# Kernel tuning notes

Measured on AMD Instinct MI355X. Metric: run time of the kernel, lower is better.

Reference implementation:

```python
import jax, jax.numpy as jnp
import numpy as np

B, D, N, MH, MV = 4, 1024, 2048, 1024, 1024

def setup_inputs() -> dict:
    key = jax.random.key(0)
    k1, k2, k3, k4, k5 = jax.random.split(key, 5)
    return {
        "x": jax.random.normal(k1, (B, D, N), dtype=jnp.float32),
        "W_Q": jax.random.normal(k2, (MH, D), dtype=jnp.float32),
        "W_K": jax.random.normal(k3, (MH, D), dtype=jnp.float32),
        "W_V": jax.random.normal(k4, (MV, D), dtype=jnp.float32),
        "W_O": jax.random.normal(k5, (D, MV), dtype=jnp.float32),
    }

def reference(x, W_Q, W_K, W_V, W_O):
    # x: [b, d, n] (feature-major). Projections: [b, m, n]
    q = jnp.einsum('hd,bdn->bhn', W_Q, x)
    k = jnp.einsum('hd,bdn->bhn', W_K, x)
    v = jnp.einsum('vd,bdn->bvn', W_V, x)
    # scores[b,i,j] = sum_h k[b,h,i] * q[b,h,j]  -> [b, n, n]; NOTE: no 1/sqrt scale (faithful)
    scores = jnp.einsum('bhi,bhj->bij', k, q)
    scores = jax.nn.softmax(scores, axis=-1)
    # v @ scores -> [b, m_V, n]
    attn = jnp.einsum('bvi,bij->bvj', v, scores)
    # W_O @ attn -> [b, d, n]
    return jnp.einsum('dv,bvj->bdj', W_O, attn)
```

## Files before the change

kernel.cpp:

```cpp
#include <hip/hip_runtime.h>
#include <cstddef>
#include <cstdint>

typedef unsigned short u16;
typedef __attribute__((ext_vector_type(8))) short bf16x8;
typedef __attribute__((ext_vector_type(8))) _Float16 f16x8;
typedef __attribute__((ext_vector_type(4))) float f32x4;
typedef __attribute__((ext_vector_type(16))) float f32x16;

#define GLOBAL_AS __attribute__((address_space(1)))
#define LDS_AS __attribute__((address_space(3)))

__device__ __forceinline__ void async16(const u16* g, u16* l) {
    __builtin_amdgcn_global_load_lds((GLOBAL_AS const uint32_t*)g,
                                     (LDS_AS uint32_t*)l, 16, 0, 0);
}

__device__ __forceinline__ u16 f2bf(float f) {
    uint32_t u = __builtin_bit_cast(uint32_t, f);
    uint32_t r = (u + 0x7FFFu + ((u >> 16) & 1u)) >> 16;
    return (u16)r;
}

__global__ __launch_bounds__(256)
void wprep(const float* __restrict__ WQ, const float* __restrict__ WK,
           const float* __restrict__ WV, const float* __restrict__ WO,
           u16* __restrict__ DQ, u16* __restrict__ DK,
           u16* __restrict__ DV, u16* __restrict__ DOb)
{
    const int role = blockIdx.z;
    __shared__ float t[32][33];
    int tx = threadIdx.x & 31, ty = threadIdx.x >> 5;
    int c0 = blockIdx.x * 32, r0 = blockIdx.y * 32;
    const float* S = role == 0 ? WQ : role == 1 ? WK : role == 2 ? WV : WO;

    if (role == 3) {
        #pragma unroll
        for (int k = 0; k < 4; ++k) {
            size_t o = (size_t)(r0 + ty + 8 * k) * 1024 + c0 + tx;
            DOb[o] = f2bf(S[o]);
        }
        return;
    }
    #pragma unroll
    for (int k = 0; k < 4; ++k)
        t[ty + 8 * k][tx] = S[(size_t)(r0 + ty + 8 * k) * 1024 + c0 + tx];
    __syncthreads();
    if (role == 2) {
        #pragma unroll
        for (int k = 0; k < 4; ++k)
            DV[(size_t)(c0 + ty + 8 * k) * 1024 + r0 + tx] = f2bf(t[tx][ty + 8 * k]);
    } else {
        u16* D = role == 0 ? DQ : DK;
        #pragma unroll
        for (int k = 0; k < 4; ++k) {
            float a = t[tx][ty + 8 * k] * 64.0f;
            _Float16 h0 = (_Float16)a;
            _Float16 h1 = (_Float16)(a - (float)h0);
            size_t o = (size_t)(c0 + ty + 8 * k) * 1024 + r0 + tx;
            D[o] = __builtin_bit_cast(u16, h0);
            D[1048576 + o] = __builtin_bit_cast(u16, h1);
        }
    }
}

__global__ __launch_bounds__(256)
void xprep(const float* __restrict__ Sb, size_t sBatch,
           u16* __restrict__ BFb, size_t bfBatch,
           u16* __restrict__ Db, size_t dBatch, size_t plane)
{
    const float* S = Sb + blockIdx.z * sBatch;
    u16* BF = BFb + blockIdx.z * bfBatch;
    u16* D = Db + blockIdx.z * dBatch;
    __shared__ float t[32][33];
    int tx = threadIdx.x & 31, ty = threadIdx.x >> 5;
    int c0 = blockIdx.x * 32, r0 = blockIdx.y * 32;
    #pragma unroll
    for (int k = 0; k < 4; ++k) {
        float v = S[(size_t)(r0 + ty + 8 * k) * 2048 + c0 + tx];
        t[ty + 8 * k][tx] = v;
        BF[(size_t)(r0 + ty + 8 * k) * 2048 + c0 + tx] = f2bf(v);
    }
    __syncthreads();
    #pragma unroll
    for (int k = 0; k < 4; ++k) {
        float a = t[tx][ty + 8 * k] * 64.0f;
        _Float16 h0 = (_Float16)a;
        _Float16 h1 = (_Float16)(a - (float)h0);
        size_t o = (size_t)(c0 + ty + 8 * k) * 1024 + r0 + tx;
        D[o] = __builtin_bit_cast(u16, h0);
        D[plane + o] = __builtin_bit_cast(u16, h1);
    }
}

#define MMF4(AF, BF)                                                                   \
    _Pragma("unroll") for (int i = 0; i < 4; ++i)                                      \
        _Pragma("unroll") for (int j = 0; j < 4; ++j)                                  \
            acc[i][j] = __builtin_amdgcn_mfma_f32_16x16x32_f16(AF[i], BF[j], acc[i][j], 0, 0, 0);
#define MMB4(AF, BF)                                                                   \
    _Pragma("unroll") for (int i = 0; i < 4; ++i)                                      \
        _Pragma("unroll") for (int j = 0; j < 4; ++j)                                  \
            acc[i][j] = __builtin_amdgcn_mfma_f32_16x16x32_bf16(AF[i], BF[j], acc[i][j], 0, 0, 0);

template<int TERMS, int SPLITK>
__global__ __launch_bounds__(256)
void gemm_big(const u16* __restrict__ Ab, size_t aPlane,
              const u16* __restrict__ Bb, size_t bPlane,
              float* __restrict__ Cb, size_t cBatch,
              int M, int N, int K)
{
    constexpr int RSZ = 4096;
    constexpr int BUF = (TERMS == 3 ? 4 : 2) * RSZ;
    __shared__ u16 lds[2 * BUF];
    const u16* A = Ab;
    const u16* B = Bb;
    const int z = blockIdx.z;
    const int kt0 = SPLITK ? z * (K >> 2) : 0;
    const int kend = SPLITK ? kt0 + (K >> 2) : K;
    const int tid = threadIdx.x;
    const int lane = tid & 63, wave = tid >> 6;
    const int m0 = blockIdx.y * 128, n0 = blockIdx.x * 128;
    const int l15 = lane & 15, q = lane >> 4;
    const int rm = (wave >> 1) * 64, rn = (wave & 1) * 64;

    int sr[2], sg[2], sbase[2];
    #pragma unroll
    for (int it = 0; it < 2; ++it) {
        int s = tid + it * 256;
        sr[it] = s >> 2;
        sg[it] = (s & 3) ^ ((sr[it] >> 1) & 3);
        sbase[it] = (it * 256 + wave * 64) * 8;
    }
    const int fsw = (q ^ ((l15 >> 1) & 3)) * 8;
    int aoff[4], boff[4];
    #pragma unroll
    for (int f = 0; f < 4; ++f) {
        aoff[f] = (rm + f * 16 + l15) * 32 + fsw;
        boff[f] = (rn + f * 16 + l15) * 32 + fsw;
    }

    f32x4 acc[4][4];
    #pragma unroll
    for (int i = 0; i < 4; ++i)
        #pragma unroll
        for (int j = 0; j < 4; ++j)
            acc[i][j] = (f32x4){0.f, 0.f, 0.f, 0.f};

#define STAGEB(PP, KT)                                                                 \
    do {                                                                               \
        _Pragma("unroll")                                                              \
        for (int it = 0; it < 2; ++it) {                                               \
            const size_t ao = (size_t)(m0 + sr[it]) * K + (KT) + sg[it] * 8;           \
            const size_t bo = (size_t)(n0 + sr[it]) * K + (KT) + sg[it] * 8;           \
            const int d = (PP) * BUF + sbase[it];                                      \
            if (TERMS == 3) {                                                          \
                async16(A + ao, &lds[d]);                                              \
                async16(A + aPlane + ao, &lds[d + RSZ]);                               \
                async16(B + bo, &lds[d + 2 * RSZ]);                                    \
                async16(B + bPlane + bo, &lds[d + 3 * RSZ]);                           \
            } else {                                                                   \
                async16(A + ao, &lds[d]);                                              \
                async16(B + bo, &lds[d + RSZ]);                                        \
            }                                                                          \
        }                                                                              \
    } while (0)

    STAGEB(0, kt0);
    for (int kt = kt0; kt < kend; kt += 32) {
        const int p = (kt >> 5) & 1;
        __syncthreads();
        if (kt + 32 < kend) STAGEB(p ^ 1, kt + 32);
        const u16* L = &lds[p * BUF];
        if (TERMS == 3) {
            f16x8 a0f[4], b0f[4], xf[4];
            #pragma unroll
            for (int f = 0; f < 4; ++f) a0f[f] = *(const f16x8*)&L[aoff[f]];
            #pragma unroll
            for (int f = 0; f < 4; ++f) b0f[f] = *(const f16x8*)&L[2 * RSZ + boff[f]];
            MMF4(a0f, b0f);
            #pragma unroll
            for (int f = 0; f < 4; ++f) xf[f] = *(const f16x8*)&L[3 * RSZ + boff[f]];
            MMF4(a0f, xf);
            #pragma unroll
            for (int f = 0; f < 4; ++f) xf[f] = *(const f16x8*)&L[RSZ + aoff[f]];
            MMF4(xf, b0f);
        } else {
            bf16x8 af[4], bf_[4];
            #pragma unroll
            for (int f = 0; f < 4; ++f) af[f] = *(const bf16x8*)&L[aoff[f]];
            #pragma unroll
            for (int f = 0; f < 4; ++f) bf_[f] = *(const bf16x8*)&L[RSZ + boff[f]];
            MMB4(af, bf_);
        }
    }
#undef STAGEB

    float* C = Cb + (size_t)z * cBatch;
    #pragma unroll
    for (int i = 0; i < 4; ++i) {
        int row = m0 + rm + i * 16 + q * 4;
        #pragma unroll
        for (int j = 0; j < 4; ++j) {
            int col = n0 + rn + j * 16 + l15;
            #pragma unroll
            for (int r = 0; r < 4; ++r)
                C[(size_t)(row + r) * N + col] = acc[i][j][r];
        }
    }
}

__global__ __launch_bounds__(256)
void reduce4b(const float4* __restrict__ P1, const float4* __restrict__ P2,
              u16* __restrict__ M2, u16* __restrict__ WOV)
{
    size_t i = blockIdx.x * 256 + threadIdx.x;
    const float4* P = blockIdx.y == 0 ? P1 : P2;
    float4 a = P[i], b = P[262144 + i], c = P[524288 + i], d = P[786432 + i];
    float v[4] = { a.x + b.x + c.x + d.x, a.y + b.y + c.y + d.y,
                   a.z + b.z + c.z + d.z, a.w + b.w + c.w + d.w };
    if (blockIdx.y == 0) {
        #pragma unroll
        for (int k = 0; k < 4; ++k) {
            float vs = v[k] * 0.000244140625f;
            _Float16 h0 = (_Float16)vs;
            _Float16 h1 = (_Float16)(vs - (float)h0);
            M2[i * 4 + k] = __builtin_bit_cast(u16, h0);
            M2[1048576 + i * 4 + k] = __builtin_bit_cast(u16, h1);
        }
    } else {
        ushort4 o = { f2bf(v[0]), f2bf(v[1]), f2bf(v[2]), f2bf(v[3]) };
        *(ushort4*)&WOV[i * 4] = o;
    }
}

#define RDAF(dst, PL, H)                                                               \
    _Pragma("unroll")                                                                  \
    for (int f = 0; f < FM; ++f)                                                       \
        dst[f] = *(const f16x8*)&L[(PL) * ASZ + arow[f] * 32 + ((2 * (H) + half) ^ asw[f]) * 8];
#define RDBF(dst, PL, H)                                                               \
    _Pragma("unroll")                                                                  \
    for (int f = 0; f < FN; ++f)                                                       \
        dst[f] = *(const f16x8*)&L[2 * ASZ + (PL) * BSZ + brow[f] * 32 + ((2 * (H) + half) ^ bsw[f]) * 8];
#define MMW(AF, BF)                                                                    \
    _Pragma("unroll")                                                                  \
    for (int i = 0; i < FM; ++i)                                                       \
        _Pragma("unroll")                                                              \
        for (int j = 0; j < FN; ++j)                                                   \
            acc[i][j] = __builtin_amdgcn_mfma_f32_32x32x16_f16(AF[i], BF[j], acc[i][j], 0, 0, 0);
#define MMWB(AF, BF)                                                                   \
    _Pragma("unroll")                                                                  \
    for (int i = 0; i < FM; ++i)                                                       \
        _Pragma("unroll")                                                              \
        for (int j = 0; j < FN; ++j)                                                   \
            acc[i][j] = __builtin_amdgcn_mfma_f32_32x32x16_bf16(AF[i], BF[j], acc[i][j], 0, 0, 0);

template<int TERMS, int EPI, int TM, int TN, int WGM, int WGN>
__global__ __launch_bounds__(512, 2)
void gemm_w(const u16* __restrict__ Ab, size_t aBatch, size_t aPlane,
            const u16* __restrict__ Bb, size_t bBatch, size_t bPlane,
            void* __restrict__ Cb, size_t cBatch, size_t cPlane,
            int M, int N, int K)
{
    constexpr int ASZ = TM * 32;
    constexpr int BSZ = TN * 32;
    constexpr int APL = (TERMS == 3) ? 2 : 1;
    constexpr int BUF = APL * (ASZ + BSZ);
    constexpr int FM = TM / WGM / 32;
    constexpr int FN = TN / WGN / 32;
    constexpr int AIT = TM / 128;
    constexpr int BIT = TN / 128;
    extern __shared__ __align__(16) u16 lds[];

    int bid = blockIdx.x + gridDim.x * blockIdx.y;
    int cpr = gridDim.x >> 2;
    int c8 = bid & 7, kk = bid >> 3;
    int bx = (kk % cpr) * 4 + (c8 & 3);
    int by = (kk / cpr) * 2 + (c8 >> 2);

    const u16* A = Ab + blockIdx.z * aBatch;
    const u16* B = Bb + blockIdx.z * bBatch;
    const int tid = threadIdx.x;
    const int lane = tid & 63, wave = tid >> 6;
    const int m0 = by * TM, n0 = bx * TN;
    const int l31 = lane & 31, half = lane >> 5;
    const int rm = (wave / WGN) * (TM / WGM);
    const int rn = (wave % WGN) * (TN / WGN);

    int arow[FM], asw[FM], brow[FN], bsw[FN];
    #pragma unroll
    for (int f = 0; f < FM; ++f) { arow[f] = rm + f * 32 + l31; asw[f] = (arow[f] >> 1) & 3; }
    #pragma unroll
    for (int f = 0; f < FN; ++f) { brow[f] = rn + f * 32 + l31; bsw[f] = (brow[f] >> 1) & 3; }

    f32x16 acc[FM][FN];
    #pragma unroll
    for (int i = 0; i < FM; ++i)
        #pragma unroll
        for (int j = 0; j < FN; ++j)
            #pragma unroll
            for (int r = 0; r < 16; ++r) acc[i][j][r] = 0.f;

    auto stage = [&](int pp, int kt) {
        #pragma unroll
        for (int it = 0; it < AIT; ++it) {
            int s = tid + it * 512;
            int r = s >> 2;
            int g = (s & 3) ^ ((r >> 1) & 3);
            int base = pp * BUF + (it * 512 + wave * 64) * 8;
            size_t go = (size_t)(m0 + r) * K + kt + g * 8;
            async16(A + go, &lds[base]);
            if (TERMS == 3) async16(A + aPlane + go, &lds[base + ASZ]);
        }
        #pragma unroll
        for (int it = 0; it < BIT; ++it) {
            int s = tid + it * 512;
            int r = s >> 2;
            int g = (s & 3) ^ ((r >> 1) & 3);
            int base = pp * BUF + APL * ASZ + (it * 512 + wave * 64) * 8;
            size_t go = (size_t)(n0 + r) * K + kt + g * 8;
            async16(B + go, &lds[base]);
            if (TERMS == 3) async16(B + bPlane + go, &lds[base + BSZ]);
        }
    };

    stage(0, 0);
    for (int kt = 0; kt < K; kt += 32) {
        const int p = (kt >> 5) & 1;
        __syncthreads();
        if (kt + 32 < K) stage(p ^ 1, kt + 32);
        const u16* L = &lds[p * BUF];
        if (TERMS == 3) {
            f16x8 A0h0[FM], A0h1[FM], B0h0[FN], B0h1[FN];
            f16x8 B1h0[FN], B1h1[FN], A1h0[FM], A1h1[FM];
            RDAF(A0h0, 0, 0) RDBF(B0h0, 0, 0)
            RDAF(A0h1, 0, 1) RDBF(B0h1, 0, 1)
            RDBF(B1h0, 1, 0)
            MMW(A0h0, B0h0)
            RDBF(B1h1, 1, 1)
            MMW(A0h1, B0h1)
            RDAF(A1h0, 1, 0)
            MMW(A0h0, B1h0)
            MMW(A0h1, B1h1)
            RDAF(A1h1, 1, 1)
            MMW(A1h0, B0h0)
            MMW(A1h1, B0h1)
        } else {
            bf16x8 Ah0[FM], Ah1[FM], Bh0[FN], Bh1[FN];
            #pragma unroll
            for (int f = 0; f < FM; ++f)
                Ah0[f] = *(const bf16x8*)&L[arow[f] * 32 + (half ^ asw[f]) * 8];
            #pragma unroll
            for (int f = 0; f < FN; ++f)
                Bh0[f] = *(const bf16x8*)&L[ASZ + brow[f] * 32 + (half ^ bsw[f]) * 8];
            #pragma unroll
            for (int f = 0; f < FM; ++f)
                Ah1[f] = *(const bf16x8*)&L[arow[f] * 32 + ((2 + half) ^ asw[f]) * 8];
            #pragma unroll
            for (int f = 0; f < FN; ++f)
                Bh1[f] = *(const bf16x8*)&L[ASZ + brow[f] * 32 + ((2 + half) ^ bsw[f]) * 8];
            MMWB(Ah0, Bh0)
            MMWB(Ah1, Bh1)
        }
    }

    #pragma unroll
    for (int i = 0; i < FM; ++i) {
        #pragma unroll
        for (int j = 0; j < FN; ++j) {
            int col = n0 + rn + j * 32 + l31;
            #pragma unroll
            for (int r = 0; r < 16; ++r) {
                int row = m0 + rm + i * 32 + (r & 3) + 8 * (r >> 2) + 4 * half;
                float v = acc[i][j][r];
                size_t o = (size_t)row * N + col;
                if (EPI == 0) {
                    ((float*)Cb + blockIdx.z * cBatch)[o] = v;
                } else if (EPI == 1) {
                    u16* C0 = (u16*)Cb + blockIdx.z * cBatch;
                    float vs = v * 0.000244140625f;
                    _Float16 h0 = (_Float16)vs;
                    _Float16 h1 = (_Float16)(vs - (float)h0);
                    C0[o] = __builtin_bit_cast(u16, h0);
                    C0[cPlane + o] = __builtin_bit_cast(u16, h1);
                } else {
                    ((u16*)Cb + blockIdx.z * cBatch)[o] = f2bf(v);
                }
            }
        }
    }
}

#undef RDAF
#undef RDBF
#undef MMW
#undef MMWB

__global__ __launch_bounds__(256)
void softmax_pt(const float* __restrict__ Sb, size_t sBatch,
                u16* __restrict__ PTb, size_t pBatch)
{
    const float* S = Sb + blockIdx.y * sBatch + (size_t)blockIdx.x * 32 * 2048;
    u16* PT = PTb + blockIdx.y * pBatch;
    const int i0 = blockIdx.x * 32;
    const int tid = threadIdx.x;
    const int row = tid >> 3, t8 = tid & 7;
    __shared__ float mrow[32], rrow[32];
    __shared__ float tbuf[32][33];

    const float* Sr = S + (size_t)row * 2048;
    float m = -3.4e38f;
    for (int c = 0; c < 64; ++c) {
        float4 x = *(const float4*)&Sr[(t8 + c * 8) * 4];
        m = fmaxf(m, fmaxf(fmaxf(x.x, x.y), fmaxf(x.z, x.w)));
    }
    #pragma unroll
    for (int off = 1; off < 8; off <<= 1)
        m = fmaxf(m, __shfl_xor(m, off, 8));
    float s = 0.f;
    for (int c = 0; c < 64; ++c) {
        float4 x = *(const float4*)&Sr[(t8 + c * 8) * 4];
        s += __expf(x.x - m) + __expf(x.y - m) + __expf(x.z - m) + __expf(x.w - m);
    }
    #pragma unroll
    for (int off = 1; off < 8; off <<= 1)
        s += __shfl_xor(s, off, 8);
    if (t8 == 0) { mrow[row] = m; rrow[row] = 1.0f / s; }

    int tx = tid & 31, ty = tid >> 5;
    for (int j0 = 0; j0 < 2048; j0 += 32) {
        __syncthreads();
        #pragma unroll
        for (int k = 0; k < 4; ++k)
            tbuf[ty + 8 * k][tx] = S[(size_t)(ty + 8 * k) * 2048 + j0 + tx];
        __syncthreads();
        float mm = mrow[tx], rr = rrow[tx];
        #pragma unroll
        for (int k = 0; k < 4; ++k) {
            float e = __expf(tbuf[tx][ty + 8 * k] - mm) * rr;
            PT[(size_t)(j0 + ty + 8 * k) * 2048 + i0 + tx] = f2bf(e);
        }
    }
}

extern "C" void kernel_launch(void* const* d_in, const int* in_sizes, int n_in,
                              void* d_out, int out_size, void* d_ws, size_t ws_size,
                              hipStream_t stream)
{
    const size_t MB = 1048576;
    const size_t WREG = 34 * MB;
    const size_t PER  = 32 * MB;
    const size_t PER_US = PER / 2, PER_F = PER / 4;

    char* ws = (char*)d_ws;
    u16* WQT2 = (u16*)ws;
    u16* WKT2 = (u16*)(ws + 4 * MB);
    u16* M2   = (u16*)(ws + 8 * MB);
    u16* WObf = (u16*)(ws + 12 * MB);
    u16* WVT  = (u16*)(ws + 14 * MB);
    u16* WOV  = (u16*)(ws + 16 * MB);
    u16* xbf  = (u16*)(ws + 18 * MB);

    int G = (ws_size >= WREG + 4 * PER) ? 4 : (ws_size >= WREG + 2 * PER) ? 2 : 1;

    const float* x = (const float*)d_in[0];
    float* out = (float*)d_out;
    dim3 blk(256);

    hipFuncSetAttribute((const void*)gemm_w<3, 0, 256, 256, 2, 4>,
                        hipFuncAttributeMaxDynamicSharedMemorySize, 131072);
    hipFuncSetAttribute((const void*)gemm_w<3, 1, 256, 128, 4, 2>,
                        hipFuncAttributeMaxDynamicSharedMemorySize, 98304);

    float* PART1 = (float*)(ws + WREG);
    float* PART2 = (float*)(ws + WREG + 16 * MB);
    wprep<<<dim3(32, 32, 4), blk, 0, stream>>>(
        (const float*)d_in[1], (const float*)d_in[2],
        (const float*)d_in[3], (const float*)d_in[4],
        WQT2, WKT2, WVT, WObf);
    gemm_big<3, 1><<<dim3(8, 8, 4), blk, 0, stream>>>(WKT2, 1048576, WQT2, 1048576,
                                                      PART1, 1048576, 1024, 1024, 1024);
    gemm_big<1, 1><<<dim3(8, 8, 4), blk, 0, stream>>>(WObf, 0, WVT, 0,
                                                      PART2, 1048576, 1024, 1024, 1024);
    reduce4b<<<dim3(1024, 2), blk, 0, stream>>>((const float4*)PART1, (const float4*)PART2,
                                                M2, WOV);

    for (int b0 = 0; b0 < 4; b0 += G) {
        char* R = ws + WREG;
        u16*   xT2 = (u16*)R;
        u16*   TT2 = (u16*)(R + 8 * MB);
        float* S32 = (float*)(R + 16 * MB);
        u16*   PTb = (u16*)(R + 8 * MB);
        u16*   XPT = (u16*)R;

        xprep<<<dim3(64, 32, G), blk, 0, stream>>>(x + (size_t)b0 * 2097152, 2097152,
                                                   xbf + (size_t)b0 * 2097152, 2097152,
                                                   xT2, PER_US, 2097152);
        gemm_w<3, 1, 256, 128, 4, 2><<<dim3(8, 8, G), 512, 98304, stream>>>(
            xT2, PER_US, 2097152, M2, 0, 1048576, TT2, PER_US, 2097152, 2048, 1024, 1024);
        gemm_w<3, 0, 256, 256, 2, 4><<<dim3(8, 8, G), 512, 131072, stream>>>(
            xT2, PER_US, 2097152, TT2, PER_US, 2097152, S32, PER_F, 0, 2048, 2048, 1024);
        softmax_pt<<<dim3(64, G), blk, 0, stream>>>(S32, PER_F, PTb, PER_US);
        gemm_w<1, 2, 256, 128, 4, 2><<<dim3(8, 8, G), 512, 49152, stream>>>(
            PTb, PER_US, 0, xbf + (size_t)b0 * 2097152, 2097152, 0,
            XPT, PER_US, 0, 2048, 1024, 2048);
        gemm_w<1, 0, 256, 128, 4, 2><<<dim3(16, 4, G), 512, 49152, stream>>>(
            WOV, 0, 0, XPT, PER_US, 0, out + (size_t)b0 * 2097152, 2097152, 0,
            1024, 2048, 1024);
    }
}
```

Before: 418.2 us.

## Fuse softmax row statistics into scores GEMM epilogue and emit transposed scores

The scores GEMM now takes its operands in swapped order, so it produces the score matrix transposed. Its epilogue also computes per-column partial max and sum-of-exp over each wave group's rows and writes them to a small stats buffer. A new texp kernel merges the 16 partial stats per column and writes the normalized bf16 probabilities with coalesced row access. This replaces the old softmax kernel, which read the scores twice and transposed them through LDS. The cost is extra exp and reduction work in the GEMM epilogue, and a stats buffer placed over workspace that earlier weight staging used.

```diff
diff --git a/kernel.cpp b/kernel.cpp
--- a/kernel.cpp
+++ b/kernel.cpp
@@ -160,7 +160,7 @@
                 async16(B + bPlane + bo, &lds[d + 3 * RSZ]);                           \
             } else {                                                                   \
                 async16(A + ao, &lds[d]);                                              \
-                async16(B + bo, &lds[d + RSZ]);                                        \
+                async16(B + bo, &lds[d + RSZ]);                                       \
             }                                                                          \
         }                                                                              \
     } while (0)
@@ -254,12 +254,12 @@
         for (int j = 0; j < FN; ++j)                                                   \
             acc[i][j] = __builtin_amdgcn_mfma_f32_32x32x16_bf16(AF[i], BF[j], acc[i][j], 0, 0, 0);
 
-template<int TERMS, int EPI, int TM, int TN, int WGM, int WGN>
+template<int TERMS, int EPI, int TM, int TN, int WGM, int WGN, int STATS>
 __global__ __launch_bounds__(512, 2)
 void gemm_w(const u16* __restrict__ Ab, size_t aBatch, size_t aPlane,
             const u16* __restrict__ Bb, size_t bBatch, size_t bPlane,
             void* __restrict__ Cb, size_t cBatch, size_t cPlane,
-            int M, int N, int K)
+            int M, int N, int K, float2* __restrict__ statsOut)
 {
     constexpr int ASZ = TM * 32;
     constexpr int BSZ = TN * 32;
@@ -363,6 +363,31 @@
         }
     }
 
+    if constexpr (STATS) {
+        #pragma unroll
+        for (int j = 0; j < FN; ++j) {
+            float mx = -3.4e38f;
+            #pragma unroll
+            for (int i = 0; i < FM; ++i)
+                #pragma unroll
+                for (int r = 0; r < 16; ++r) mx = fmaxf(mx, acc[i][j][r]);
+            float se = 0.f;
+            #pragma unroll
+            for (int i = 0; i < FM; ++i)
+                #pragma unroll
+                for (int r = 0; r < 16; ++r) se += __expf(acc[i][j][r] - mx);
+            float mo = __shfl_xor(mx, 32, 64);
+            float so = __shfl_xor(se, 32, 64);
+            float mM = fmaxf(mx, mo);
+            float sS = se * __expf(mx - mM) + so * __expf(mo - mM);
+            if (half == 0) {
+                int col = n0 + rn + j * 32 + l31;
+                int grp = by * WGM + (wave / WGN);
+                statsOut[((size_t)blockIdx.z * 16 + grp) * 2048 + col] = (float2){mM, sS};
+            }
+        }
+    }
+
     #pragma unroll
     for (int i = 0; i < FM; ++i) {
         #pragma unroll
@@ -396,49 +421,45 @@
 #undef MMWB
 
 __global__ __launch_bounds__(256)
-void softmax_pt(const float* __restrict__ Sb, size_t sBatch,
-                u16* __restrict__ PTb, size_t pBatch)
-{
-    const float* S = Sb + blockIdx.y * sBatch + (size_t)blockIdx.x * 32 * 2048;
+void texp(const float* __restrict__ STb, size_t sBatch,
+          const float2* __restrict__ SG, u16* __restrict__ PTb, size_t pBatch)
+{
+    const float* ST = STb + blockIdx.y * sBatch;
     u16* PT = PTb + blockIdx.y * pBatch;
-    const int i0 = blockIdx.x * 32;
-    const int tid = threadIdx.x;
-    const int row = tid >> 3, t8 = tid & 7;
-    __shared__ float mrow[32], rrow[32];
-    __shared__ float tbuf[32][33];
-
-    const float* Sr = S + (size_t)row * 2048;
-    float m = -3.4e38f;
-    for (int c = 0; c < 64; ++c) {
-        float4 x = *(const float4*)&Sr[(t8 + c * 8) * 4];
-        m = fmaxf(m, fmaxf(fmaxf(x.x, x.y), fmaxf(x.z, x.w)));
-    }
-    #pragma unroll
-    for (int off = 1; off < 8; off <<= 1)
-        m = fmaxf(m, __shfl_xor(m, off, 8));
-    float s = 0.f;
-    for (int c = 0; c < 64; ++c) {
-        float4 x = *(const float4*)&Sr[(t8 + c * 8) * 4];
-        s += __expf(x.x - m) + __expf(x.y - m) + __expf(x.z - m) + __expf(x.w - m);
-    }
-    #pragma unroll
-    for (int off = 1; off < 8; off <<= 1)
-        s += __shfl_xor(s, off, 8);
-    if (t8 == 0) { mrow[row] = m; rrow[row] = 1.0f / s; }
-
-    int tx = tid & 31, ty = tid >> 5;
-    for (int j0 = 0; j0 < 2048; j0 += 32) {
-        __syncthreads();
-        #pragma unroll
-        for (int k = 0; k < 4; ++k)
-            tbuf[ty + 8 * k][tx] = S[(size_t)(ty + 8 * k) * 2048 + j0 + tx];
-        __syncthreads();
-        float mm = mrow[tx], rr = rrow[tx];
-        #pragma unroll
-        for (int k = 0; k < 4; ++k) {
-            float e = __expf(tbuf[tx][ty + 8 * k] - mm) * rr;
-            PT[(size_t)(j0 + ty + 8 * k) * 2048 + i0 + tx] = f2bf(e);
-        }
+    const float2* st = SG + (size_t)blockIdx.y * 16 * 2048;
+    const int t = threadIdx.x;
+
+    float Mv[8], Rv[8];
+    #pragma unroll
+    for (int e = 0; e < 8; ++e) {
+        int col = (e < 4) ? (4 * t + e) : (1024 + 4 * t + (e - 4));
+        float M = -3.4e38f, S = 0.f;
+        #pragma unroll
+        for (int g = 0; g < 16; ++g) {
+            float2 p = st[g * 2048 + col];
+            if (p.x > M) { S = S * __expf(M - p.x) + p.y; M = p.x; }
+            else         { S += p.y * __expf(p.x - M); }
+        }
+        Mv[e] = M;
+        Rv[e] = 1.0f / S;
+    }
+
+    const int j0 = blockIdx.x * 16;
+    for (int jr = 0; jr < 16; ++jr) {
+        const float* row = ST + (size_t)(j0 + jr) * 2048;
+        u16* prow = PT + (size_t)(j0 + jr) * 2048;
+        float4 v0 = *(const float4*)&row[4 * t];
+        float4 v1 = *(const float4*)&row[1024 + 4 * t];
+        ushort4 o0 = { f2bf(__expf(v0.x - Mv[0]) * Rv[0]),
+                       f2bf(__expf(v0.y - Mv[1]) * Rv[1]),
+                       f2bf(__expf(v0.z - Mv[2]) * Rv[2]),
+                       f2bf(__expf(v0.w - Mv[3]) * Rv[3]) };
+        ushort4 o1 = { f2bf(__expf(v1.x - Mv[4]) * Rv[4]),
+                       f2bf(__expf(v1.y - Mv[5]) * Rv[5]),
+                       f2bf(__expf(v1.z - Mv[6]) * Rv[6]),
+                       f2bf(__expf(v1.w - Mv[7]) * Rv[7]) };
+        *(ushort4*)&prow[4 * t] = o0;
+        *(ushort4*)&prow[1024 + 4 * t] = o1;
     }
 }
 
@@ -459,6 +480,7 @@
     u16* WVT  = (u16*)(ws + 14 * MB);
     u16* WOV  = (u16*)(ws + 16 * MB);
     u16* xbf  = (u16*)(ws + 18 * MB);
+    float2* STATSG = (float2*)ws;
 
     int G = (ws_size >= WREG + 4 * PER) ? 4 : (ws_size >= WREG + 2 * PER) ? 2 : 1;
 
@@ -466,9 +488,9 @@
     float* out = (float*)d_out;
     dim3 blk(256);
 
-    hipFuncSetAttribute((const void*)gemm_w<3, 0, 256, 256, 2, 4>,
+    hipFuncSetAttribute((const void*)gemm_w<3, 0, 256, 256, 2, 4, 1>,
                         hipFuncAttributeMaxDynamicSharedMemorySize, 131072);
-    hipFuncSetAttribute((const void*)gemm_w<3, 1, 256, 128, 4, 2>,
+    hipFuncSetAttribute((const void*)gemm_w<3, 1, 256, 128, 4, 2, 0>,
                         hipFuncAttributeMaxDynamicSharedMemorySize, 98304);
 
     float* PART1 = (float*)(ws + WREG);
@@ -488,23 +510,25 @@
         char* R = ws + WREG;
         u16*   xT2 = (u16*)R;
         u16*   TT2 = (u16*)(R + 8 * MB);
-        float* S32 = (float*)(R + 16 * MB);
+        float* ST  = (float*)(R + 16 * MB);
         u16*   PTb = (u16*)(R + 8 * MB);
         u16*   XPT = (u16*)R;
 
         xprep<<<dim3(64, 32, G), blk, 0, stream>>>(x + (size_t)b0 * 2097152, 2097152,
                                                    xbf + (size_t)b0 * 2097152, 2097152,
                                                    xT2, PER_US, 2097152);
-        gemm_w<3, 1, 256, 128, 4, 2><<<dim3(8, 8, G), 512, 98304, stream>>>(
-            xT2, PER_US, 2097152, M2, 0, 1048576, TT2, PER_US, 2097152, 2048, 1024, 1024);
-        gemm_w<3, 0, 256, 256, 2, 4><<<dim3(8, 8, G), 512, 131072, stream>>>(
-            xT2, PER_US, 2097152, TT2, PER_US, 2097152, S32, PER_F, 0, 2048, 2048, 1024);
-        softmax_pt<<<dim3(64, G), blk, 0, stream>>>(S32, PER_F, PTb, PER_US);
-        gemm_w<1, 2, 256, 128, 4, 2><<<dim3(8, 8, G), 512, 49152, stream>>>(
+        gemm_w<3, 1, 256, 128, 4, 2, 0><<<dim3(8, 8, G), 512, 98304, stream>>>(
+            xT2, PER_US, 2097152, M2, 0, 1048576, TT2, PER_US, 2097152,
+            2048, 1024, 1024, nullptr);
+        gemm_w<3, 0, 256, 256, 2, 4, 1><<<dim3(8, 8, G), 512, 131072, stream>>>(
+            TT2, PER_US, 2097152, xT2, PER_US, 2097152, ST, PER_F, 0,
+            2048, 2048, 1024, STATSG);
+        texp<<<dim3(128, G), blk, 0, stream>>>(ST, PER_F, STATSG, PTb, PER_US);
+        gemm_w<1, 2, 256, 128, 4, 2, 0><<<dim3(8, 8, G), 512, 49152, stream>>>(
             PTb, PER_US, 0, xbf + (size_t)b0 * 2097152, 2097152, 0,
-            XPT, PER_US, 0, 2048, 1024, 2048);
-        gemm_w<1, 0, 256, 128, 4, 2><<<dim3(16, 4, G), 512, 49152, stream>>>(
+            XPT, PER_US, 0, 2048, 1024, 2048, nullptr);
+        gemm_w<1, 0, 256, 128, 4, 2, 0><<<dim3(16, 4, G), 512, 49152, stream>>>(
             WOV, 0, 0, XPT, PER_US, 0, out + (size_t)b0 * 2097152, 2097152, 0,
-            1024, 2048, 1024);
-    }
-}
+            1024, 2048, 1024, nullptr);
+    }
+}
```

Result: faster. 403.2 us (-3.6%).
